# Kernel tuning notes

Hardware: AMD Instinct MI355X
Metric: run time of the kernel (lower is better)

## Reference

```python
import jax, jax.numpy as jnp
import numpy as np

TRACE_LR = 0.1
TRACE_DECAY = 0.99
ERASE_LR = 1.0
EPS = 1e-8


def setup_inputs() -> dict:
    key = jax.random.key(0)
    k1, k2, k3, k4 = jax.random.split(key, 4)
    B, H, S, D = 8, 8, 4096, 64
    DM = 768
    Q = jax.random.normal(k1, (B, H, S, D), dtype=jnp.float32)
    V = jax.random.normal(k2, (B, H, S, D), dtype=jnp.float32)
    # value_traces buffer (small random state so erase path is non-trivial)
    trace = jax.random.normal(k3, (H, D, D), dtype=jnp.float32) * 0.01
    # W_out: Linear(H*D -> DM), weight shape (DM, H*D), out = x @ W.T
    W_out = jax.random.normal(k4, (DM, H * D), dtype=jnp.float32) / np.sqrt(H * D)
    return {"Q": Q, "V": V, "trace": trace, "W_out": W_out}


def _hebbian_write(Q, V, trace):
    """Erase-before-write + decayed Hebbian outer-product update.

    Q, V: (B, H, S, D); trace: (H, D, D). Shift-1 offset: key at i, value at i+2.
    """
    B, H, S, D = Q.shape
    Q_store = Q[:, :, :-2, :]            # (B,H,S-2,D)
    V_store = V[:, :, 2:, :]             # (B,H,S-2,D)
    denom = B * (S - 2)
    # reconsolidation erasure of old associations along normalized keys
    Q_norm = jnp.clip(jnp.linalg.norm(Q_store, axis=-1, keepdims=True), EPS)
    Q_erase = Q_store / Q_norm
    V_old = jnp.einsum('bhip,hpq->bhiq', Q_erase, trace)
    erase = jnp.einsum('bhip,bhiq->hpq', Q_erase, V_old) / denom
    trace = trace - ERASE_LR * erase
    # Hebbian outer-product write
    update = jnp.einsum('bhip,bhiq->hpq', Q_store, V_store) / denom
    return TRACE_DECAY * trace + TRACE_LR * update


def reference(Q, V, trace, W_out):
    B, H, S, D = Q.shape
    new_trace = _hebbian_write(Q, V, trace)
    # shift-1 retrieval: Q_addr at position i uses Q from position i-1
    Q_addr = jnp.concatenate(
        [jnp.zeros_like(Q[:, :, :1, :]), Q[:, :, :-1, :]], axis=2)  # (B,H,S,D)
    V_ret = jnp.einsum('bhsp,hpq->bhsq', Q_addr, new_trace)          # (B,H,S,D)
    V_ret = V_ret.transpose(0, 2, 1, 3).reshape(B, S, H * D)         # (B,S,H*D)
    return V_ret @ W_out.T                                           # (B,S,d_model)
```

## Files before the change

### kernel.cpp

```cpp
#include <hip/hip_runtime.h>

#define B_ 8
#define H_ 8
#define S_ 4096
#define D_ 64
#define DM_ 768
#define NSTORE 4094
#define DENOM 32752.0f

typedef short bfrag_t __attribute__((ext_vector_type(8)));
typedef float f32x4_t __attribute__((ext_vector_type(4)));

__device__ inline unsigned short f2bf(float x) {
    unsigned int u = __float_as_uint(x);
    unsigned int r = (u + 0x7fffu + ((u >> 16) & 1u)) >> 16;
    return (unsigned short)r;
}

__device__ inline void async_copy16(const void* g, void* lds) {
    __builtin_amdgcn_global_load_lds((__attribute__((address_space(1))) void*)g,
                                     (__attribute__((address_space(3))) void*)lds,
                                     16, 0, 0);
}

#define MFMA16(a, b, c) __builtin_amdgcn_mfma_f32_16x16x32_bf16((a), (b), (c), 0, 0, 0)

template <bool PART>
__global__ __launch_bounds__(256, 4) void gram_kernel(
    const float* __restrict__ Q, const float* __restrict__ V,
    float* __restrict__ gG, float* __restrict__ gU,
    unsigned short* __restrict__ Qbf, float* __restrict__ gP, int writeQbf) {
    const int split = blockIdx.x, h = blockIdx.y, b = blockIdx.z;
    const int nsplit = gridDim.x;
    const int rowsPer = 4096 / nsplit;
    const int nTiles = rowsPer >> 6;
    const int t = threadIdx.x;
    const int wave = t >> 6, lane = t & 63;
    const int quad = lane >> 4, l15 = lane & 15;
    __shared__ __align__(16) unsigned short QT[64 * 64];
    __shared__ __align__(16) unsigned short QnT[64 * 64];
    __shared__ __align__(16) unsigned short VT[64 * 64];

    const size_t bh = (size_t)(b * H_ + h);
    const float* Qbh = Q + bh * S_ * D_;
    const float* Vbh = V + bh * S_ * D_;
    unsigned short* Qo = Qbf + bh * S_ * D_;

    f32x4_t accG[4] = {}, accU[4] = {};
    const int r0 = split * rowsPer;

    for (int tile = 0; tile < nTiles; ++tile) {
        const int rbase = r0 + tile * 64;
        #pragma unroll
        for (int i = 0; i < 4; ++i) {
            int f = i * 256 + t;
            int rowl = f >> 4, c4 = f & 15;
            int r = rbase + rowl;
            float4 q4 = *(const float4*)(Qbh + (size_t)r * D_ + c4 * 4);
            if (writeQbf) {
                ushort4 u;
                u.x = f2bf(q4.x); u.y = f2bf(q4.y); u.z = f2bf(q4.z); u.w = f2bf(q4.w);
                *(ushort4*)(Qo + (size_t)r * D_ + c4 * 4) = u;
            }
            float4 v4 = make_float4(0.f, 0.f, 0.f, 0.f);
            if (r < NSTORE) v4 = *(const float4*)(Vbh + (size_t)(r + 2) * D_ + c4 * 4);
            else q4 = make_float4(0.f, 0.f, 0.f, 0.f);
            float ss = q4.x * q4.x + q4.y * q4.y + q4.z * q4.z + q4.w * q4.w;
            ss += __shfl_xor(ss, 1);
            ss += __shfl_xor(ss, 2);
            ss += __shfl_xor(ss, 4);
            ss += __shfl_xor(ss, 8);
            float sc = 1.0f / fmaxf(ss, 1e-16f);
            int col = rowl ^ ((c4 & 7) << 3);
            float qa[4] = {q4.x, q4.y, q4.z, q4.w};
            float va[4] = {v4.x, v4.y, v4.z, v4.w};
            #pragma unroll
            for (int j = 0; j < 4; ++j) {
                int p = c4 * 4 + j;
                QT [p * 64 + col] = f2bf(qa[j]);
                QnT[p * 64 + col] = f2bf(qa[j] * sc);
                VT [p * 64 + col] = f2bf(va[j]);
            }
        }
        __syncthreads();
        #pragma unroll
        for (int c = 0; c < 2; ++c) {
            int pA = wave * 16 + l15;
            int offA = pA * 64 + (((c * 4 + quad) ^ ((pA >> 2) & 7)) << 3);
            bfrag_t ag = *(const bfrag_t*)&QnT[offA];
            bfrag_t au = *(const bfrag_t*)&QT[offA];
            #pragma unroll
            for (int j = 0; j < 4; ++j) {
                int pB = j * 16 + l15;
                int offB = pB * 64 + (((c * 4 + quad) ^ ((pB >> 2) & 7)) << 3);
                bfrag_t bq = *(const bfrag_t*)&QT[offB];
                bfrag_t bv = *(const bfrag_t*)&VT[offB];
                accG[j] = MFMA16(ag, bq, accG[j]);
                accU[j] = MFMA16(au, bv, accU[j]);
            }
        }
        __syncthreads();
    }
    if (PART) {
        const int slab = split * 8 + b;
        float* base = gP + ((size_t)(h * 128 + slab) * 2) * 4096;
        #pragma unroll
        for (int j = 0; j < 4; ++j) {
            int coln = j * 16 + l15;
            #pragma unroll
            for (int r = 0; r < 4; ++r) {
                int row = wave * 16 + quad * 4 + r;
                base[row * 64 + coln]        = accG[j][r];
                base[4096 + row * 64 + coln] = accU[j][r];
            }
        }
    } else {
        float* gGh = gG + h * 4096;
        float* gUh = gU + h * 4096;
        #pragma unroll
        for (int j = 0; j < 4; ++j) {
            int coln = j * 16 + l15;
            #pragma unroll
            for (int r = 0; r < 4; ++r) {
                int row = wave * 16 + quad * 4 + r;
                atomicAdd(&gGh[row * 64 + coln], accG[j][r]);
                atomicAdd(&gUh[row * 64 + coln], accU[j][r]);
            }
        }
    }
}

__global__ __launch_bounds__(256) void reduce_kernel(
    const float* __restrict__ gP, float* __restrict__ gG, float* __restrict__ gU) {
    const int h = blockIdx.x, chunk = blockIdx.y, t = threadIdx.x;
    const int arr = t >> 7, idx = chunk * 128 + (t & 127);
    const float* base = gP + ((size_t)(h * 128) * 2 + arr) * 4096 + idx;
    float s = 0.f;
    #pragma unroll 8
    for (int sl = 0; sl < 128; ++sl) s += base[(size_t)sl * 2 * 4096];
    (arr ? gU : gG)[h * 4096 + idx] = s;
}

__global__ __launch_bounds__(256) void trace_kernel(
    const float* __restrict__ gG, const float* __restrict__ gU,
    const float* __restrict__ trace, float* __restrict__ Tnew) {
    const int h = blockIdx.x, t = threadIdx.x;
    __shared__ float Gs[64][68];
    __shared__ float Ts[64][68];
    const float* Gh = gG + h * 4096;
    const float* Uh = gU + h * 4096;
    const float* Th = trace + h * 4096;
    float* To = Tnew + h * 4096;
    for (int k = 0; k < 16; ++k) {
        int e = k * 256 + t;
        Gs[e >> 6][e & 63] = Gh[e];
        Ts[e >> 6][e & 63] = Th[e];
    }
    __syncthreads();
    const int p = t >> 2, q0 = (t & 3) * 16;
    f32x4_t acc[4] = {};
    for (int r = 0; r < 64; ++r) {
        float g = Gs[p][r];
        #pragma unroll
        for (int i = 0; i < 4; ++i) {
            f32x4_t tv = *(const f32x4_t*)&Ts[r][q0 + i * 4];
            acc[i] += g * tv;
        }
    }
    const float inv = 1.0f / DENOM;
    #pragma unroll
    for (int i = 0; i < 4; ++i) {
        int e = p * 64 + q0 + i * 4;
        f32x4_t ts = *(const f32x4_t*)&Ts[p][q0 + i * 4];
        f32x4_t uu = *(const f32x4_t*)(Uh + e);
        f32x4_t res = 0.99f * (ts - acc[i] * inv) + (0.1f * inv) * uu;
        *(f32x4_t*)(To + e) = res;
    }
}

__global__ __launch_bounds__(256) void wc_kernel(
    const float* __restrict__ Tnew, const float* __restrict__ Wout,
    unsigned short* __restrict__ WcT) {
    const int nc = blockIdx.x, h = blockIdx.y, t = threadIdx.x;
    __shared__ float TsT[64][68];
    __shared__ float WbT[64][132];
    const float* Th = Tnew + h * 4096;
    #pragma unroll
    for (int i = 0; i < 4; ++i) {
        int f = i * 256 + t;
        int p = f >> 4, q4 = f & 15;
        float4 v = *(const float4*)(Th + p * 64 + q4 * 4);
        TsT[q4 * 4 + 0][p] = v.x; TsT[q4 * 4 + 1][p] = v.y;
        TsT[q4 * 4 + 2][p] = v.z; TsT[q4 * 4 + 3][p] = v.w;
    }
    #pragma unroll
    for (int i = 0; i < 8; ++i) {
        int f = i * 256 + t;
        int n = f >> 4, q4 = f & 15;
        float4 w = *(const float4*)(Wout + (size_t)(nc * 128 + n) * 512 + h * 64 + q4 * 4);
        WbT[q4 * 4 + 0][n] = w.x; WbT[q4 * 4 + 1][n] = w.y;
        WbT[q4 * 4 + 2][n] = w.z; WbT[q4 * 4 + 3][n] = w.w;
    }
    __syncthreads();
    const int n0 = (t >> 4) * 8, p0 = (t & 15) * 4;
    f32x4_t acc[8] = {};
    for (int q = 0; q < 64; ++q) {
        f32x4_t tp = *(const f32x4_t*)&TsT[q][p0];
        f32x4_t w0 = *(const f32x4_t*)&WbT[q][n0];
        f32x4_t w1 = *(const f32x4_t*)&WbT[q][n0 + 4];
        #pragma unroll
        for (int i = 0; i < 4; ++i) acc[i] += w0[i] * tp;
        #pragma unroll
        for (int i = 0; i < 4; ++i) acc[4 + i] += w1[i] * tp;
    }
    #pragma unroll
    for (int i = 0; i < 8; ++i) {
        int n = nc * 128 + n0 + i;
        ushort4 u;
        u.x = f2bf(acc[i][0]); u.y = f2bf(acc[i][1]);
        u.z = f2bf(acc[i][2]); u.w = f2bf(acc[i][3]);
        *(ushort4*)(WcT + (size_t)n * 512 + h * 64 + p0) = u;
    }
}

__global__ __launch_bounds__(256, 3) void matmul_fast(
    const unsigned short* __restrict__ Qb, const unsigned short* __restrict__ WcT,
    float* __restrict__ out) {
    const int mTile = blockIdx.x;
    const int nTile = blockIdx.y;
    const int t = threadIdx.x;
    const int wave = t >> 6, lane = t & 63;
    const int wm = wave >> 1, wn = wave & 1;
    const int quad = lane >> 4, l15 = lane & 15;
    __shared__ __align__(16) unsigned short As[128 * 64];
    __shared__ __align__(16) unsigned short Bs[128 * 64];
    const int b = mTile >> 5;
    const int s0 = (mTile & 31) * 128;
    const int nBase = nTile * 128;
    const int rl8 = lane >> 3, g = lane & 7;
    const int gs = g ^ rl8;
    f32x4_t acc[4][4] = {};

    for (int h = 0; h < 8; ++h) {
        const unsigned short* Qbh = Qb + (size_t)(b * H_ + h) * S_ * D_;
        #pragma unroll
        for (int k = 0; k < 4; ++k) {
            int ch = wave * 4 + k;
            int row = ch * 8 + rl8;
            int s = s0 + row;
            int sc = (s > 0) ? (s - 1) : 0;
            async_copy16(Qbh + (size_t)sc * 64 + gs * 8, &As[ch * 512 + lane * 8]);
            async_copy16(WcT + (size_t)(nBase + row) * 512 + h * 64 + gs * 8,
                         &Bs[ch * 512 + lane * 8]);
        }
        __syncthreads();
        if (s0 == 0) {
            if (t < 8) ((uint4*)As)[t] = make_uint4(0, 0, 0, 0);
            __syncthreads();
        }
        #pragma unroll
        for (int c = 0; c < 2; ++c) {
            int gk = c * 4 + quad;
            bfrag_t af[4], bf[4];
            #pragma unroll
            for (int i = 0; i < 4; ++i) {
                int row = wm * 64 + i * 16 + l15;
                af[i] = *(const bfrag_t*)&As[row * 64 + ((gk ^ (row & 7)) << 3)];
            }
            #pragma unroll
            for (int j = 0; j < 4; ++j) {
                int row = wn * 64 + j * 16 + l15;
                bf[j] = *(const bfrag_t*)&Bs[row * 64 + ((gk ^ (row & 7)) << 3)];
            }
            #pragma unroll
            for (int i = 0; i < 4; ++i)
                #pragma unroll
                for (int j = 0; j < 4; ++j)
                    acc[i][j] = MFMA16(af[i], bf[j], acc[i][j]);
        }
        __syncthreads();
    }
    const size_t mBase = (size_t)mTile * 128;
    #pragma unroll
    for (int i = 0; i < 4; ++i) {
        int mrow = wm * 64 + i * 16 + quad * 4;
        #pragma unroll
        for (int j = 0; j < 4; ++j) {
            int n = nBase + wn * 64 + j * 16 + l15;
            #pragma unroll
            for (int r = 0; r < 4; ++r)
                out[(mBase + mrow + r) * DM_ + n] = acc[i][j][r];
        }
    }
}

__global__ __launch_bounds__(256, 2) void matmul_f32(
    const float* __restrict__ Qf, const unsigned short* __restrict__ WcT,
    float* __restrict__ out) {
    const int mTile = blockIdx.x, nTile = blockIdx.y;
    const int t = threadIdx.x;
    const int wave = t >> 6, lane = t & 63;
    const int wm = wave >> 1, wn = wave & 1;
    const int quad = lane >> 4, l15 = lane & 15;
    __shared__ __align__(16) unsigned short As[128][72];
    __shared__ __align__(16) unsigned short Bs[128][72];
    const int b = mTile >> 5;
    const int s0 = (mTile & 31) * 128;
    const int nBase = nTile * 128;
    f32x4_t acc[4][4] = {};
    for (int h = 0; h < 8; ++h) {
        const float* Qbh = Qf + (size_t)(b * H_ + h) * S_ * D_;
        #pragma unroll
        for (int i = 0; i < 8; ++i) {
            int f = i * 256 + t;
            int row = f >> 4, c4 = f & 15;
            int s = s0 + row;
            float4 q4 = make_float4(0.f, 0.f, 0.f, 0.f);
            if (s > 0) q4 = *(const float4*)(Qbh + (size_t)(s - 1) * D_ + c4 * 4);
            ushort4 u;
            u.x = f2bf(q4.x); u.y = f2bf(q4.y); u.z = f2bf(q4.z); u.w = f2bf(q4.w);
            *(ushort4*)(&As[row][c4 * 4]) = u;
        }
        #pragma unroll
        for (int i = 0; i < 4; ++i) {
            int f = i * 256 + t;
            int row = f >> 3, c8 = f & 7;
            uint4 w = *(const uint4*)(WcT + (size_t)(nBase + row) * 512 + h * 64 + c8 * 8);
            *(uint4*)(&Bs[row][c8 * 8]) = w;
        }
        __syncthreads();
        #pragma unroll
        for (int c = 0; c < 2; ++c) {
            int k0 = c * 32 + quad * 8;
            bfrag_t af[4], bf[4];
            #pragma unroll
            for (int i = 0; i < 4; ++i)
                af[i] = *(const bfrag_t*)(&As[wm * 64 + i * 16 + l15][k0]);
            #pragma unroll
            for (int j = 0; j < 4; ++j)
                bf[j] = *(const bfrag_t*)(&Bs[wn * 64 + j * 16 + l15][k0]);
            #pragma unroll
            for (int i = 0; i < 4; ++i)
                #pragma unroll
                for (int j = 0; j < 4; ++j)
                    acc[i][j] = MFMA16(af[i], bf[j], acc[i][j]);
        }
        __syncthreads();
    }
    const size_t mBase = (size_t)mTile * 128;
    #pragma unroll
    for (int i = 0; i < 4; ++i) {
        int mrow = wm * 64 + i * 16 + quad * 4;
        #pragma unroll
        for (int j = 0; j < 4; ++j) {
            int n = nBase + wn * 64 + j * 16 + l15;
            #pragma unroll
            for (int r = 0; r < 4; ++r)
                out[(mBase + mrow + r) * DM_ + n] = acc[i][j][r];
        }
    }
}

extern "C" void kernel_launch(void* const* d_in, const int* in_sizes, int n_in,
                              void* d_out, int out_size, void* d_ws, size_t ws_size,
                              hipStream_t stream) {
    const float* Q     = (const float*)d_in[0];
    const float* V     = (const float*)d_in[1];
    const float* trace = (const float*)d_in[2];
    const float* Wout  = (const float*)d_in[3];
    float* out = (float*)d_out;

    float* gG   = (float*)d_ws;
    float* gU   = gG + 32768;
    float* Tnew = gU + 32768;
    unsigned short* WcT = (unsigned short*)(Tnew + 32768);
    unsigned short* Qbf = WcT + 393216;
    float* gP = (float*)(Qbf + (size_t)B_ * H_ * S_ * D_);

    const size_t needQbf  = 1179648u + 33554432u;
    const size_t needFull = needQbf + 33554432u;
    const int mode = (ws_size >= needFull) ? 2 : ((ws_size >= needQbf) ? 1 : 0);

    if (mode == 2) {
        gram_kernel<true><<<dim3(16, 8, 8), 256, 0, stream>>>(Q, V, gG, gU, Qbf, gP, 1);
        reduce_kernel<<<dim3(8, 32), 256, 0, stream>>>(gP, gG, gU);
    } else {
        hipMemsetAsync(d_ws, 0, 2 * 32768 * sizeof(float), stream);
        gram_kernel<false><<<dim3(8, 8, 8), 256, 0, stream>>>(Q, V, gG, gU, Qbf, gP, mode >= 1);
    }
    trace_kernel<<<8, 256, 0, stream>>>(gG, gU, trace, Tnew);
    wc_kernel<<<dim3(6, 8), 256, 0, stream>>>(Tnew, Wout, WcT);
    if (mode >= 1)
        matmul_fast<<<dim3(256, 6), 256, 0, stream>>>(Qbf, WcT, out);
    else
        matmul_f32<<<dim3(256, 6), 256, 0, stream>>>(Q, WcT, out);
}
```

Before: 267.0 us.

## Double-buffer gram tiles with register prefetch and scaled-Q single buffer

Rewrites the gram kernel's tile loop. Global loads for the next tile are prefetched into registers, and LDS is double-buffered, which removes the second barrier per tile. It stores Q scaled by 1/||q|| and V scaled by ||q|| in one shared Q buffer, so both Gram products reuse a single A fragment and one LDS array is dropped. It also uses DPP reductions, permlane swaps, and packed bf16 converts to cut shuffle and store cost. The trade-offs are a changed rounding pattern (the scaling is folded into V) and extra register pressure from the prefetched tiles.

```diff
diff --git a/kernel.cpp b/kernel.cpp
--- a/kernel.cpp
+++ b/kernel.cpp
@@ -15,6 +15,25 @@
     unsigned int u = __float_as_uint(x);
     unsigned int r = (u + 0x7fffu + ((u >> 16) & 1u)) >> 16;
     return (unsigned short)r;
+}
+
+__device__ inline unsigned int cvtpk(float lo, float hi) {
+    unsigned int r;
+    asm("v_cvt_pk_bf16_f32 %0, %1, %2" : "=v"(r) : "v"(lo), "v"(hi));
+    return r;
+}
+
+__device__ inline void pl16swap(float& a, float& b) {
+    asm("v_permlane16_swap_b32 %0, %1" : "+v"(a), "+v"(b));
+}
+__device__ inline void pl32swap(float& a, float& b) {
+    asm("v_permlane32_swap_b32 %0, %1" : "+v"(a), "+v"(b));
+}
+
+template <int CTRL>
+__device__ inline float dpp_add(float x) {
+    int y = __builtin_amdgcn_update_dpp(0, __float_as_int(x), CTRL, 0xf, 0xf, true);
+    return x + __int_as_float(y);
 }
 
 __device__ inline void async_copy16(const void* g, void* lds) {
@@ -37,9 +56,10 @@
     const int t = threadIdx.x;
     const int wave = t >> 6, lane = t & 63;
     const int quad = lane >> 4, l15 = lane & 15;
-    __shared__ __align__(16) unsigned short QT[64 * 64];
-    __shared__ __align__(16) unsigned short QnT[64 * 64];
-    __shared__ __align__(16) unsigned short VT[64 * 64];
+    const int rgrp = t >> 4;
+    const int c4 = t & 15;
+    __shared__ __align__(16) unsigned short Qs[2][4096];
+    __shared__ __align__(16) unsigned short Vs[2][4096];
 
     const size_t bh = (size_t)(b * H_ + h);
     const float* Qbh = Q + bh * S_ * D_;
@@ -49,57 +69,74 @@
     f32x4_t accG[4] = {}, accU[4] = {};
     const int r0 = split * rowsPer;
 
+    float4 qr[4], vr[4];
+    auto loadT = [&](int tile) {
+        const int rbase = r0 + tile * 64;
+        #pragma unroll
+        for (int i = 0; i < 4; ++i) {
+            int r = rbase + i * 16 + rgrp;
+            qr[i] = *(const float4*)(Qbh + (size_t)r * D_ + c4 * 4);
+            vr[i] = (r < NSTORE) ? *(const float4*)(Vbh + (size_t)(r + 2) * D_ + c4 * 4)
+                                 : make_float4(0.f, 0.f, 0.f, 0.f);
+        }
+    };
+    auto rd8 = [&](const unsigned short* arr, int p, int gk) {
+        const int bx = p & 15;
+        uint2 lo = *(const uint2*)&arr[p * 64 + (((gk * 2) ^ bx) << 2)];
+        uint2 hi = *(const uint2*)&arr[p * 64 + (((gk * 2 + 1) ^ bx) << 2)];
+        union { uint2 u2[2]; bfrag_t f; } u;
+        u.u2[0] = lo; u.u2[1] = hi;
+        return u.f;
+    };
+
+    loadT(0);
     for (int tile = 0; tile < nTiles; ++tile) {
+        const int buf = tile & 1;
         const int rbase = r0 + tile * 64;
+        unsigned short* Qb_ = Qs[buf];
+        unsigned short* Vb_ = Vs[buf];
         #pragma unroll
         for (int i = 0; i < 4; ++i) {
-            int f = i * 256 + t;
-            int rowl = f >> 4, c4 = f & 15;
-            int r = rbase + rowl;
-            float4 q4 = *(const float4*)(Qbh + (size_t)r * D_ + c4 * 4);
+            int r = rbase + i * 16 + rgrp;
+            float4 q4 = qr[i], v4 = vr[i];
             if (writeQbf) {
-                ushort4 u;
-                u.x = f2bf(q4.x); u.y = f2bf(q4.y); u.z = f2bf(q4.z); u.w = f2bf(q4.w);
-                *(ushort4*)(Qo + (size_t)r * D_ + c4 * 4) = u;
-            }
-            float4 v4 = make_float4(0.f, 0.f, 0.f, 0.f);
-            if (r < NSTORE) v4 = *(const float4*)(Vbh + (size_t)(r + 2) * D_ + c4 * 4);
-            else q4 = make_float4(0.f, 0.f, 0.f, 0.f);
+                uint2 u = make_uint2(cvtpk(q4.x, q4.y), cvtpk(q4.z, q4.w));
+                *(uint2*)(Qo + (size_t)r * D_ + c4 * 4) = u;
+            }
+            if (r >= NSTORE) q4 = make_float4(0.f, 0.f, 0.f, 0.f);
             float ss = q4.x * q4.x + q4.y * q4.y + q4.z * q4.z + q4.w * q4.w;
-            ss += __shfl_xor(ss, 1);
-            ss += __shfl_xor(ss, 2);
-            ss += __shfl_xor(ss, 4);
-            ss += __shfl_xor(ss, 8);
-            float sc = 1.0f / fmaxf(ss, 1e-16f);
-            int col = rowl ^ ((c4 & 7) << 3);
-            float qa[4] = {q4.x, q4.y, q4.z, q4.w};
-            float va[4] = {v4.x, v4.y, v4.z, v4.w};
+            ss = dpp_add<0xB1>(ss);
+            ss = dpp_add<0x4E>(ss);
+            ss = dpp_add<0x141>(ss);
+            ss = dpp_add<0x140>(ss);
+            float sc = fmaxf(ss, 1e-16f);
+            float sr = rsqrtf(sc);
+            float sv = sc * sr;
+            float a0 = q4.x * sr, a1 = q4.y * sr, a2 = q4.z * sr, a3 = q4.w * sr;
+            float b0 = v4.x * sv, b1 = v4.y * sv, b2 = v4.z * sv, b3 = v4.w * sv;
+            pl16swap(a0, a1); pl16swap(a2, a3);
+            pl32swap(a0, a2); pl32swap(a1, a3);
+            pl16swap(b0, b1); pl16swap(b2, b3);
+            pl32swap(b0, b2); pl32swap(b1, b3);
+            const int p = c4 * 4 + quad;
+            const int off = p * 64 + (((i * 4 + wave) ^ (p & 15)) << 2);
+            *(uint2*)&Qb_[off] = make_uint2(cvtpk(a0, a1), cvtpk(a2, a3));
+            *(uint2*)&Vb_[off] = make_uint2(cvtpk(b0, b1), cvtpk(b2, b3));
+        }
+        if (tile + 1 < nTiles) loadT(tile + 1);
+        __syncthreads();
+        #pragma unroll
+        for (int c = 0; c < 2; ++c) {
+            const int gk = c * 4 + quad;
+            bfrag_t af = rd8(Qb_, wave * 16 + l15, gk);
             #pragma unroll
             for (int j = 0; j < 4; ++j) {
-                int p = c4 * 4 + j;
-                QT [p * 64 + col] = f2bf(qa[j]);
-                QnT[p * 64 + col] = f2bf(qa[j] * sc);
-                VT [p * 64 + col] = f2bf(va[j]);
-            }
-        }
-        __syncthreads();
-        #pragma unroll
-        for (int c = 0; c < 2; ++c) {
-            int pA = wave * 16 + l15;
-            int offA = pA * 64 + (((c * 4 + quad) ^ ((pA >> 2) & 7)) << 3);
-            bfrag_t ag = *(const bfrag_t*)&QnT[offA];
-            bfrag_t au = *(const bfrag_t*)&QT[offA];
-            #pragma unroll
-            for (int j = 0; j < 4; ++j) {
-                int pB = j * 16 + l15;
-                int offB = pB * 64 + (((c * 4 + quad) ^ ((pB >> 2) & 7)) << 3);
-                bfrag_t bq = *(const bfrag_t*)&QT[offB];
-                bfrag_t bv = *(const bfrag_t*)&VT[offB];
-                accG[j] = MFMA16(ag, bq, accG[j]);
-                accU[j] = MFMA16(au, bv, accU[j]);
-            }
-        }
-        __syncthreads();
+                bfrag_t bq = rd8(Qb_, j * 16 + l15, gk);
+                bfrag_t bv = rd8(Vb_, j * 16 + l15, gk);
+                accG[j] = MFMA16(af, bq, accG[j]);
+                accU[j] = MFMA16(af, bv, accU[j]);
+            }
+        }
     }
     if (PART) {
         const int slab = split * 8 + b;
```

Result: no change. 266.8 us (-0.0%).
